# Kernel tuning notes

Hardware: AMD Instinct MI355X
Metric: run time of the kernel (lower is better)

The kernel has to match this reference:

```python
import jax, jax.numpy as jnp
import numpy as np
import math

B, H, L = 8, 512, 2048
CH = 1          # channels
D2 = 32         # d_state // 2 (conjugate pairs)
DT_MIN, DT_MAX = 0.001, 0.1


def setup_inputs() -> dict:
    key = jax.random.key(0)
    ks = jax.random.split(key, 7)
    u = jax.random.normal(ks[0], (B, H, L), dtype=jnp.float32)
    # Chebyshev initialization (SimpleS4)
    h_scale = jnp.exp(jnp.arange(H, dtype=jnp.float32) / H * math.log(DT_MAX / DT_MIN))
    angles = jnp.arange(D2, dtype=jnp.float32) * jnp.pi
    theta = jnp.broadcast_to(angles[None, None, :], (CH, H, D2)).astype(jnp.float32) + 0.0
    a = -(jnp.broadcast_to(h_scale[None, :, None], (CH, H, D2)).astype(jnp.float32) + 0.0)
    b = jax.random.normal(ks[1], (CH, H, D2), dtype=jnp.float32)
    c = jax.random.normal(ks[2], (CH, H, D2), dtype=jnp.float32)
    x0 = jax.random.normal(ks[3], (CH, H, D2), dtype=jnp.float32)
    D = jax.random.normal(ks[4], (CH, H), dtype=jnp.float32)
    lim = 1.0 / math.sqrt(CH * H)
    W = jax.random.uniform(ks[5], (H, CH * H), minval=-lim, maxval=lim, dtype=jnp.float32)
    bias = jax.random.uniform(ks[6], (H,), minval=-lim, maxval=lim, dtype=jnp.float32)
    return dict(u=u, a=a, theta=theta, b=b, c=c, x0=x0, D=D, W=W, bias=bias)


def fft_conv(u, f):
    # u: (B,H,L), f: (C,H,L) -> causal conv (B,C,H,L) via zero-padded FFT
    n = 2 * u.shape[-1]
    u_f = jnp.fft.rfft(u, n=n)
    f_f = jnp.fft.rfft(f, n=n)
    y = jnp.fft.irfft(jnp.einsum('bhl,chl->bchl', u_f, f_f), n=n)
    return y[..., : u.shape[-1]]


def s4_forward(u, a, theta, b, c, x0, D, W, bias):
    Bsz, Hd, l = u.shape
    T = 1.0 / (l - 1)                                   # quadrature step
    z = T * jnp.arange(l, dtype=u.dtype)                # (L,)
    aa = -jnp.abs(a)                                    # (C,H,D2) stable decay
    # Vandermonde-like basis: exp(a z) cos(theta z), shape (C,H,D2,L)
    base = jnp.exp(aa[..., None] * z) * jnp.cos(theta[..., None] * z)
    q = b * c                                           # (C,H,D2)
    f = 2.0 * T * jnp.einsum('chd,chdl->chl', q, base)  # SSM kernel (C,H,L)
    y = fft_conv(u, f)                                  # (B,C,H,L)
    # trapezoid-rule endpoint correction
    y = y - 0.5 * (jnp.einsum('ch,bhl->bchl', f[:, :, 0], u)
                   + jnp.einsum('chl,bh->bchl', f, u[:, :, 0]))
    # initial-state contribution (x0 term)
    k0 = 2.0 * jnp.einsum('chd,chdl->chl', c * x0, base)
    y = y + k0[None]
    # skip connection D*u
    y = y + jnp.einsum('ch,bhl->bchl', D, u)
    y = y.reshape(Bsz, CH * Hd, l)                      # (B, C*H, L)
    # NonLinear head: GELU -> pointwise Linear(C*H -> H) (transposed conv1x1)
    y = jax.nn.gelu(y, approximate=False)
    out = jnp.einsum('hf,bfl->bhl', W, y) + bias[None, :, None]
    return out


def reference(u, a, theta, b, c, x0, D, W, bias):
    return s4_forward(u, a, theta, b, c, x0, D, W, bias)
```

## Files before the change

### kernel.cpp

```cpp
#include <hip/hip_runtime.h>
#include <hip/hip_bf16.h>

#define B_  8
#define H_  512
#define L_  2048
#define D2_ 32
#define NC_ 64
#define LC_ 32
#define EP  36

typedef __attribute__((ext_vector_type(8))) short short8;
typedef __attribute__((ext_vector_type(8))) _Float16 half8;
typedef __attribute__((ext_vector_type(2))) _Float16 half2v;
typedef __attribute__((ext_vector_type(4))) float float4v;

__device__ __forceinline__ half2v pk_fma16(half2v a, half2v b, half2v c) {
    return __builtin_elementwise_fma(a, b, c);
}

__device__ __forceinline__ float gelu_fast(float x) {
    float q = x * fmaf(0.044715f, x * x, 1.0f);
    float s = __expf(-1.5957691216057308f * q);
    return __fdividef(x, 1.0f + s);
}

__device__ __forceinline__ unsigned pack_bf16x2(float x, float y) {
    __hip_bfloat162 p = __float22bfloat162_rn(make_float2(x, y));
    return *(unsigned*)&p;
}
__device__ __forceinline__ float2 unpack_bf16x2(unsigned v) {
    __hip_bfloat162 p = *(__hip_bfloat162*)&v;
    return __bfloat1622float2(p);
}
__device__ __forceinline__ unsigned pack_f16x2(float x, float y) {
    auto v = __builtin_amdgcn_cvt_pkrtz(x, y);
    return *(unsigned*)&v;
}

__device__ __forceinline__ void load_lds16(const void* g, void* l) {
    __builtin_amdgcn_global_load_lds((const __attribute__((address_space(1))) unsigned int*)g,
                                     (__attribute__((address_space(3))) unsigned int*)l, 16, 0, 0);
}

__global__ void cast_prep_kernel(const float* __restrict__ W, __hip_bfloat16* __restrict__ Wb,
                                 const float* __restrict__ a, const float* __restrict__ th,
                                 const float* __restrict__ bb, const float* __restrict__ cc,
                                 const float* __restrict__ x0,
                                 float* __restrict__ aT, float* __restrict__ thT,
                                 float* __restrict__ qT, float* __restrict__ gxT,
                                 _Float16* __restrict__ WPh) {
    int tid = blockIdx.x * 256 + threadIdx.x;
    Wb[tid] = __float2bfloat16(W[tid]);
    if (tid < H_ * D2_) {
        int h = tid & (H_ - 1);
        int d = tid >> 9;
        const float T = 1.0f / (float)(L_ - 1);
        float av = -fabsf(a[h * D2_ + d]);
        float tv = th[h * D2_ + d];
        float q  = bb[h * D2_ + d] * cc[h * D2_ + d];
        aT[tid]  = av;
        thT[tid] = tv;
        qT[tid]  = q;
        gxT[tid] = 2.0f * cc[h * D2_ + d] * x0[h * D2_ + d];
        #pragma unroll
        for (int k = 0; k < 6; ++k) {
            float len = (float)(32 << k);
            float e2  = __expf(av * T * len);
            float an  = tv * T * len;
            WPh[((size_t)h * 6 + k) * 64 + d]      = (_Float16)(e2 * __cosf(an));
            WPh[((size_t)h * 6 + k) * 64 + 32 + d] = (_Float16)(e2 * __sinf(an));
        }
    }
}

__global__ __launch_bounds__(256) void fkprep_kernel(
        const float* __restrict__ aT, const float* __restrict__ thT,
        const float* __restrict__ qT, const float* __restrict__ gxT,
        unsigned* __restrict__ FKf, _Float16* __restrict__ AB,
        _Float16* __restrict__ CB) {
    __shared__ float f_lds[32];
    int h = blockIdx.x;
    int t = threadIdx.x;
    int q4 = t & 3, lc = t >> 2;
    const float T = 1.0f / (float)(L_ - 1);
    float z0 = T * (float)(lc * 32);
    float pr[8], pi[8], wr[8], wi[8], qd[8], gx[8];
    #pragma unroll
    for (int j = 0; j < 8; ++j) {
        int idx = (q4 * 8 + j) * H_ + h;
        float aa = aT[idx], tv = thT[idx];
        float e0 = __expf(aa * z0);
        pr[j] = e0 * __cosf(tv * z0);
        pi[j] = e0 * __sinf(tv * z0);
        float e1 = __expf(aa * T);
        wr[j] = e1 * __cosf(tv * T);
        wi[j] = e1 * __sinf(tv * T);
        qd[j] = qT[idx];
        gx[j] = gxT[idx];
    }
    for (int i = 0; i < 32; ++i) {
        float fa = 0.f, ka = 0.f;
        #pragma unroll
        for (int j = 0; j < 8; ++j) {
            fa = fmaf(qd[j], pr[j], fa);
            ka = fmaf(gx[j], pr[j], ka);
            float nr = fmaf(pr[j], wr[j], -(pi[j] * wi[j]));
            float ni = fmaf(pr[j], wi[j],  (pi[j] * wr[j]));
            pr[j] = nr; pi[j] = ni;
        }
        fa += __shfl_xor(fa, 1); fa += __shfl_xor(fa, 2);
        ka += __shfl_xor(ka, 1); ka += __shfl_xor(ka, 2);
        if (q4 == 0) {
            float fv = 2.0f * T * fa;
            FKf[(size_t)h * L_ + lc * 32 + i] = pack_bf16x2(fv, ka);
            if (lc == 0) f_lds[i] = fv;
        }
    }
    __syncthreads();
    for (int e = t; e < 64 * 32; e += 256) {
        int m = e >> 5, i = e & 31;
        int d = m & 31;
        float av = aT[d * H_ + h], tv = thT[d * H_ + h];
        float z  = T * (float)(31 - i);
        float ex = __expf(av * z);
        float v  = (m < 32) ? ex * __cosf(tv * z) : ex * __sinf(tv * z);
        AB[(size_t)h * 2048 + e] = (_Float16)v;
    }
    for (int e = t; e < 32 * 96; e += 256) {
        int i = e / 96, k = e - i * 96;
        float v = 0.f;
        if (k < 32) {
            if (k <= i) v = f_lds[i - k];
        } else {
            int d = (k < 64) ? k - 32 : k - 64;
            float av = aT[d * H_ + h], tv = thT[d * H_ + h];
            float qs = 2.0f * T * qT[d * H_ + h];
            float z  = T * (float)(i + 1);
            float ex = __expf(av * z);
            v = (k < 64) ? qs * ex * __cosf(tv * z) : -qs * ex * __sinf(tv * z);
        }
        CB[(size_t)h * 3072 + e] = (_Float16)v;
    }
}

__global__ __launch_bounds__(128, 6) void scan_mfma_kernel(
        const float* __restrict__ u, const _Float16* __restrict__ AB,
        const _Float16* __restrict__ CB, const unsigned* __restrict__ WPh,
        const float* __restrict__ Dp, const unsigned* __restrict__ FKf,
        __hip_bfloat16* __restrict__ y) {
    __shared__ __align__(16) unsigned El[64 * EP];
    int wid = threadIdx.x >> 6, lane = threadIdx.x & 63;
    int h = blockIdx.x, b = blockIdx.y;
    int ln = lane & 15, qq = lane >> 4;
    const float* ug = u + (size_t)(b * H_ + h) * L_;

    half8 uf[4];
    #pragma unroll
    for (int nb = 0; nb < 4; ++nb) {
        const float* p = ug + (nb * 16 + ln) * 32 + qq * 8;
        float4 a0 = *(const float4*)p;
        float4 a1 = *(const float4*)(p + 4);
        unsigned* vp = (unsigned*)&uf[nb];
        vp[0] = pack_f16x2(a0.x, a0.y);
        vp[1] = pack_f16x2(a0.z, a0.w);
        vp[2] = pack_f16x2(a1.x, a1.y);
        vp[3] = pack_f16x2(a1.z, a1.w);
    }

    const _Float16* ABh = AB + (size_t)h * 2048;
    int j0 = wid * 8 + qq * 2;
    #pragma unroll
    for (int e = 0; e < 2; ++e) {
        half8 af = *(const half8*)&ABh[(e * 32 + wid * 16 + ln) * 32 + qq * 8];
        #pragma unroll
        for (int nb = 0; nb < 4; ++nb) {
            float4v acc = (float4v){0.f, 0.f, 0.f, 0.f};
            acc = __builtin_amdgcn_mfma_f32_16x16x32_f16(af, uf[nb], acc, 0, 0, 0);
            unsigned p0 = pack_f16x2(acc[0], acc[1]);
            unsigned p1 = pack_f16x2(acc[2], acc[3]);
            *(uint2*)&El[(nb * 16 + ln) * EP + e * 16 + j0] = make_uint2(p0, p1);
        }
    }
    asm volatile("s_waitcnt lgkmcnt(0)" ::: "memory");
    __builtin_amdgcn_sched_barrier(0);

    int c = lane;
    unsigned sr[8], si[8];
    {
        const unsigned* rp = &El[c * EP + wid * 8];
        uint4 r0 = *(const uint4*)rp;
        uint4 r1 = *(const uint4*)(rp + 4);
        uint4 i0 = *(const uint4*)(rp + 16);
        uint4 i1 = *(const uint4*)(rp + 20);
        sr[0]=r0.x; sr[1]=r0.y; sr[2]=r0.z; sr[3]=r0.w;
        sr[4]=r1.x; sr[5]=r1.y; sr[6]=r1.z; sr[7]=r1.w;
        si[0]=i0.x; si[1]=i0.y; si[2]=i0.z; si[3]=i0.w;
        si[4]=i1.x; si[5]=i1.y; si[6]=i1.z; si[7]=i1.w;
    }
    const unsigned* mpb = WPh + (size_t)h * 6 * 32;
    #pragma unroll
    for (int st = 0; st < 6; ++st) {
        int off = 1 << st;
        int src = (c - off) & 63;
        bool act = c >= off;
        const unsigned* mp = mpb + st * 32 + wid * 8;
        #pragma unroll
        for (int jj = 0; jj < 8; ++jj) {
            unsigned prp = (unsigned)__shfl((int)sr[jj], src);
            unsigned pip = (unsigned)__shfl((int)si[jj], src);
            if (!act) { prp = 0u; pip = 0u; }
            unsigned mru = mp[jj];
            unsigned miu = mp[16 + jj];
            unsigned min_ = miu ^ 0x80008000u;
            half2v pr = *(half2v*)&prp, pi = *(half2v*)&pip;
            half2v Mr = *(half2v*)&mru, Mi = *(half2v*)&miu, Mni = *(half2v*)&min_;
            half2v s_r = *(half2v*)&sr[jj], s_i = *(half2v*)&si[jj];
            half2v nr = pk_fma16(pr, Mr, pk_fma16(pi, Mni, s_r));
            half2v ni = pk_fma16(pr, Mi, pk_fma16(pi, Mr,  s_i));
            sr[jj] = *(unsigned*)&nr; si[jj] = *(unsigned*)&ni;
        }
    }
    {
        int srcm1 = (c - 1) & 63;
        #pragma unroll
        for (int jj = 0; jj < 8; ++jj) {
            unsigned a0 = (unsigned)__shfl((int)sr[jj], srcm1);
            unsigned b0 = (unsigned)__shfl((int)si[jj], srcm1);
            if (c == 0) { a0 = 0u; b0 = 0u; }
            sr[jj] = a0; si[jj] = b0;
        }
    }
    {
        unsigned* wp = &El[c * EP + wid * 8];
        *(uint4*)wp        = make_uint4(sr[0], sr[1], sr[2], sr[3]);
        *(uint4*)(wp + 4)  = make_uint4(sr[4], sr[5], sr[6], sr[7]);
        *(uint4*)(wp + 16) = make_uint4(si[0], si[1], si[2], si[3]);
        *(uint4*)(wp + 20) = make_uint4(si[4], si[5], si[6], si[7]);
    }
    const unsigned* fgh = FKf + (size_t)h * L_;
    uint4 fkp[2][2];
    #pragma unroll
    for (int nbi = 0; nbi < 2; ++nbi) {
        int col = (2 * wid + nbi) * 16 + ln;
        fkp[nbi][0] = *(const uint4*)&fgh[col * 32 + qq * 4];
        fkp[nbi][1] = *(const uint4*)&fgh[col * 32 + 16 + qq * 4];
    }
    __syncthreads();

    const _Float16* CBh = CB + (size_t)h * 3072;
    float4v acc2[2][2];
    #pragma unroll
    for (int mb = 0; mb < 2; ++mb)
        #pragma unroll
        for (int nbi = 0; nbi < 2; ++nbi)
            acc2[mb][nbi] = (float4v){0.f, 0.f, 0.f, 0.f};
    #pragma unroll
    for (int ks = 0; ks < 3; ++ks) {
        half8 a2[2];
        a2[0] = *(const half8*)&CBh[(ln)      * 96 + ks * 32 + qq * 8];
        a2[1] = *(const half8*)&CBh[(16 + ln) * 96 + ks * 32 + qq * 8];
        #pragma unroll
        for (int nbi = 0; nbi < 2; ++nbi) {
            int col = (2 * wid + nbi) * 16 + ln;
            half8 bfv;
            if (ks == 0) bfv = uf[2 * wid + nbi];
            else {
                int off = (ks == 1) ? 0 : 16;
                bfv = *(const half8*)&El[col * EP + off + qq * 4];
            }
            acc2[0][nbi] = __builtin_amdgcn_mfma_f32_16x16x32_f16(a2[0], bfv, acc2[0][nbi], 0, 0, 0);
            acc2[1][nbi] = __builtin_amdgcn_mfma_f32_16x16x32_f16(a2[1], bfv, acc2[1][nbi], 0, 0, 0);
        }
    }

    float f0; { f0 = unpack_bf16x2(fgh[0]).x; }
    float c0v = Dp[h] - 0.5f * f0;
    float c1v = -0.5f * ug[0];
    #pragma unroll
    for (int nbi = 0; nbi < 2; ++nbi) {
        int col = (2 * wid + nbi) * 16 + ln;
        #pragma unroll
        for (int mb = 0; mb < 2; ++mb) {
            int l0 = col * 32 + mb * 16 + qq * 4;
            float4 u4 = *(const float4*)(ug + l0);
            uint4 fkv = fkp[nbi][mb];
            float us[4] = {u4.x, u4.y, u4.z, u4.w};
            unsigned fs[4] = {fkv.x, fkv.y, fkv.z, fkv.w};
            float g[4];
            #pragma unroll
            for (int r = 0; r < 4; ++r) {
                float2 fk = unpack_bf16x2(fs[r]);
                float yv = acc2[mb][nbi][r] + fmaf(c0v, us[r], fmaf(c1v, fk.x, fk.y));
                g[r] = gelu_fast(yv);
            }
            uint2 yo;
            yo.x = pack_bf16x2(g[0], g[1]);
            yo.y = pack_bf16x2(g[2], g[3]);
            *(uint2*)((short*)y + (size_t)(b * H_ + h) * L_ + l0) = yo;
        }
    }
}

__global__ __launch_bounds__(256) void transpose_y_kernel(
        const __hip_bfloat16* __restrict__ y, __hip_bfloat16* __restrict__ yT) {
    __shared__ short tile[64][72];
    int l0 = blockIdx.x * 64, f0 = blockIdx.y * 64, b = blockIdx.z;
    int t = threadIdx.x;
    int row = t >> 3, col8 = (t & 7) * 8;
    const short* yg = (const short*)y + (size_t)b * H_ * L_;
    #pragma unroll
    for (int r2 = 0; r2 < 64; r2 += 32)
        *(uint4*)&tile[row + r2][col8] =
            *(const uint4*)&yg[(size_t)(f0 + row + r2) * L_ + l0 + col8];
    __syncthreads();
    short* og = (short*)yT + (size_t)b * L_ * H_;
    #pragma unroll
    for (int r2 = 0; r2 < 64; r2 += 32) {
        int lrow = row + r2;
        short v[8];
        #pragma unroll
        for (int j = 0; j < 8; ++j) v[j] = tile[col8 + j][lrow];
        *(uint4*)&og[(size_t)(l0 + lrow) * H_ + f0 + col8] = *(uint4*)v;
    }
}

__global__ __launch_bounds__(256) void gemm_kernel(
        const __hip_bfloat16* __restrict__ Wb, const __hip_bfloat16* __restrict__ yT,
        const float* __restrict__ bias, float* __restrict__ out) {
    __shared__ __align__(16) short As[64 * 32];
    __shared__ __align__(16) short Bs[128 * 32];
    int l0 = blockIdx.x * 128;
    int h0 = blockIdx.y * 64;
    int b  = blockIdx.z;
    int t    = threadIdx.x;
    int lane = t & 63, wave = t >> 6;
    int m_off = (wave >> 1) * 32, n_off = (wave & 1) * 64;
    int quad = lane >> 4, ln = lane & 15;

    float4v acc[2][4];
    #pragma unroll
    for (int mt = 0; mt < 2; ++mt)
        #pragma unroll
        for (int nt = 0; nt < 4; ++nt)
            acc[mt][nt] = (float4v){0.f, 0.f, 0.f, 0.f};

    const short* Wg = (const short*)Wb;
    const short* Yg = (const short*)(yT + (size_t)b * L_ * H_);

    int r  = t >> 2;
    int qd = t & 3;

    for (int kt = 0; kt < 16; ++kt) {
        int k0 = kt * 32;
        load_lds16(Wg + (h0 + r) * 512 + k0 + qd * 8, &As[t * 8]);
        load_lds16(Yg + (size_t)(l0 + r)      * 512 + k0 + qd * 8, &Bs[t * 8]);
        load_lds16(Yg + (size_t)(l0 + r + 64) * 512 + k0 + qd * 8, &Bs[(t + 256) * 8]);
        __syncthreads();

        short8 af[2], bf[4];
        #pragma unroll
        for (int mt = 0; mt < 2; ++mt)
            af[mt] = *(const short8*)&As[(m_off + mt * 16 + ln) * 32 + quad * 8];
        #pragma unroll
        for (int nt = 0; nt < 4; ++nt)
            bf[nt] = *(const short8*)&Bs[(n_off + nt * 16 + ln) * 32 + quad * 8];
        #pragma unroll
        for (int mt = 0; mt < 2; ++mt)
            #pragma unroll
            for (int nt = 0; nt < 4; ++nt)
                acc[mt][nt] = __builtin_amdgcn_mfma_f32_16x16x32_bf16(
                    af[mt], bf[nt], acc[mt][nt], 0, 0, 0);
        __syncthreads();
    }

    #pragma unroll
    for (int mt = 0; mt < 2; ++mt) {
        #pragma unroll
        for (int nt = 0; nt < 4; ++nt) {
            int hh = h0 + m_off + mt * 16 + quad * 4;
            int ll = l0 + n_off + nt * 16 + ln;
            #pragma unroll
            for (int r2 = 0; r2 < 4; ++r2)
                out[((size_t)(b * H_ + hh + r2)) * L_ + ll] = acc[mt][nt][r2] + bias[hh + r2];
        }
    }
}

extern "C" void kernel_launch(void* const* d_in, const int* in_sizes, int n_in,
                              void* d_out, int out_size, void* d_ws, size_t ws_size,
                              hipStream_t stream) {
    const float* u    = (const float*)d_in[0];
    const float* a    = (const float*)d_in[1];
    const float* th   = (const float*)d_in[2];
    const float* bb   = (const float*)d_in[3];
    const float* cc   = (const float*)d_in[4];
    const float* x0   = (const float*)d_in[5];
    const float* Dp   = (const float*)d_in[6];
    const float* W    = (const float*)d_in[7];
    const float* bias = (const float*)d_in[8];
    float* out = (float*)d_out;
    char* ws = (char*)d_ws;

    unsigned*       FKf = (unsigned*)ws;
    __hip_bfloat16* yT  = (__hip_bfloat16*)(ws + (4ull  << 20));
    __hip_bfloat16* y   = (__hip_bfloat16*)(ws + (20ull << 20));
    __hip_bfloat16* Wb  = (__hip_bfloat16*)(ws + (36ull << 20));
    _Float16*       AB  = (_Float16*)(ws + (37ull << 20));
    _Float16*       CB  = (_Float16*)(ws + (39ull << 20));
    float* pbase = (float*)(ws + (42ull << 20));
    float *aT  = pbase,           *thT = pbase + 16384, *qT = pbase + 2*16384,
          *gxT = pbase + 3*16384;
    _Float16* WPh = (_Float16*)(pbase + 4*16384);

    hipLaunchKernelGGL(cast_prep_kernel,  dim3(1024),      dim3(256), 0, stream,
                       W, Wb, a, th, bb, cc, x0, aT, thT, qT, gxT, WPh);
    hipLaunchKernelGGL(fkprep_kernel,     dim3(H_),        dim3(256), 0, stream,
                       aT, thT, qT, gxT, FKf, AB, CB);
    hipLaunchKernelGGL(scan_mfma_kernel,  dim3(H_, B_),    dim3(128), 0, stream,
                       u, AB, CB, (const unsigned*)WPh, Dp, FKf, y);
    hipLaunchKernelGGL(transpose_y_kernel,dim3(32, 8, 8),  dim3(256), 0, stream, y, yT);
    hipLaunchKernelGGL(gemm_kernel,       dim3(16, 8, 8),  dim3(256), 0, stream,
                       Wb, yT, bias, out);
}
```

Before: 171.9 us.

## Process two batches per scan block and XOR-swizzle transpose LDS tile

The scan kernel now handles two batch elements per block, reusing the per-channel AB/CB matrices, scan multipliers and FK loads across both batches and halving the grid. Launch bounds drop to 4 waves to leave room for the doubled register state. Separately, the transpose kernel XOR-swizzles its shared tile columns so the column-wise reads hit fewer LDS bank conflicts. The trade-off is higher register and LDS use per block and fewer blocks in flight for latency hiding.

```diff
diff --git a/kernel.cpp b/kernel.cpp
--- a/kernel.cpp
+++ b/kernel.cpp
@@ -143,28 +143,34 @@
     }
 }
 
-__global__ __launch_bounds__(128, 6) void scan_mfma_kernel(
+__global__ __launch_bounds__(128, 4) void scan_mfma_kernel(
         const float* __restrict__ u, const _Float16* __restrict__ AB,
         const _Float16* __restrict__ CB, const unsigned* __restrict__ WPh,
         const float* __restrict__ Dp, const unsigned* __restrict__ FKf,
         __hip_bfloat16* __restrict__ y) {
-    __shared__ __align__(16) unsigned El[64 * EP];
+    __shared__ __align__(16) unsigned El[2][64 * EP];
     int wid = threadIdx.x >> 6, lane = threadIdx.x & 63;
-    int h = blockIdx.x, b = blockIdx.y;
+    int h = blockIdx.x, b0 = blockIdx.y * 2;
     int ln = lane & 15, qq = lane >> 4;
-    const float* ug = u + (size_t)(b * H_ + h) * L_;
-
-    half8 uf[4];
-    #pragma unroll
-    for (int nb = 0; nb < 4; ++nb) {
-        const float* p = ug + (nb * 16 + ln) * 32 + qq * 8;
-        float4 a0 = *(const float4*)p;
-        float4 a1 = *(const float4*)(p + 4);
-        unsigned* vp = (unsigned*)&uf[nb];
-        vp[0] = pack_f16x2(a0.x, a0.y);
-        vp[1] = pack_f16x2(a0.z, a0.w);
-        vp[2] = pack_f16x2(a1.x, a1.y);
-        vp[3] = pack_f16x2(a1.z, a1.w);
+    const float* ug[2] = { u + (size_t)(b0 * H_ + h) * L_,
+                           u + (size_t)((b0 + 1) * H_ + h) * L_ };
+
+    half8 uf[2][4];
+    float u0[2];
+    #pragma unroll
+    for (int bi = 0; bi < 2; ++bi) {
+        u0[bi] = ug[bi][0];
+        #pragma unroll
+        for (int nb = 0; nb < 4; ++nb) {
+            const float* p = ug[bi] + (nb * 16 + ln) * 32 + qq * 8;
+            float4 a0 = *(const float4*)p;
+            float4 a1 = *(const float4*)(p + 4);
+            unsigned* vp = (unsigned*)&uf[bi][nb];
+            vp[0] = pack_f16x2(a0.x, a0.y);
+            vp[1] = pack_f16x2(a0.z, a0.w);
+            vp[2] = pack_f16x2(a1.x, a1.y);
+            vp[3] = pack_f16x2(a1.z, a1.w);
+        }
     }
 
     const _Float16* ABh = AB + (size_t)h * 2048;
@@ -173,29 +179,31 @@
     for (int e = 0; e < 2; ++e) {
         half8 af = *(const half8*)&ABh[(e * 32 + wid * 16 + ln) * 32 + qq * 8];
         #pragma unroll
-        for (int nb = 0; nb < 4; ++nb) {
-            float4v acc = (float4v){0.f, 0.f, 0.f, 0.f};
-            acc = __builtin_amdgcn_mfma_f32_16x16x32_f16(af, uf[nb], acc, 0, 0, 0);
-            unsigned p0 = pack_f16x2(acc[0], acc[1]);
-            unsigned p1 = pack_f16x2(acc[2], acc[3]);
-            *(uint2*)&El[(nb * 16 + ln) * EP + e * 16 + j0] = make_uint2(p0, p1);
-        }
+        for (int bi = 0; bi < 2; ++bi)
+            #pragma unroll
+            for (int nb = 0; nb < 4; ++nb) {
+                float4v acc = (float4v){0.f, 0.f, 0.f, 0.f};
+                acc = __builtin_amdgcn_mfma_f32_16x16x32_f16(af, uf[bi][nb], acc, 0, 0, 0);
+                *(uint2*)&El[bi][(nb * 16 + ln) * EP + e * 16 + j0] =
+                    make_uint2(pack_f16x2(acc[0], acc[1]), pack_f16x2(acc[2], acc[3]));
+            }
     }
     asm volatile("s_waitcnt lgkmcnt(0)" ::: "memory");
     __builtin_amdgcn_sched_barrier(0);
 
     int c = lane;
-    unsigned sr[8], si[8];
-    {
-        const unsigned* rp = &El[c * EP + wid * 8];
+    unsigned sr[2][8], si[2][8];
+    #pragma unroll
+    for (int bi = 0; bi < 2; ++bi) {
+        const unsigned* rp = &El[bi][c * EP + wid * 8];
         uint4 r0 = *(const uint4*)rp;
         uint4 r1 = *(const uint4*)(rp + 4);
         uint4 i0 = *(const uint4*)(rp + 16);
         uint4 i1 = *(const uint4*)(rp + 20);
-        sr[0]=r0.x; sr[1]=r0.y; sr[2]=r0.z; sr[3]=r0.w;
-        sr[4]=r1.x; sr[5]=r1.y; sr[6]=r1.z; sr[7]=r1.w;
-        si[0]=i0.x; si[1]=i0.y; si[2]=i0.z; si[3]=i0.w;
-        si[4]=i1.x; si[5]=i1.y; si[6]=i1.z; si[7]=i1.w;
+        sr[bi][0]=r0.x; sr[bi][1]=r0.y; sr[bi][2]=r0.z; sr[bi][3]=r0.w;
+        sr[bi][4]=r1.x; sr[bi][5]=r1.y; sr[bi][6]=r1.z; sr[bi][7]=r1.w;
+        si[bi][0]=i0.x; si[bi][1]=i0.y; si[bi][2]=i0.z; si[bi][3]=i0.w;
+        si[bi][4]=i1.x; si[bi][5]=i1.y; si[bi][6]=i1.z; si[bi][7]=i1.w;
     }
     const unsigned* mpb = WPh + (size_t)h * 6 * 32;
     #pragma unroll
@@ -206,36 +214,42 @@
         const unsigned* mp = mpb + st * 32 + wid * 8;
         #pragma unroll
         for (int jj = 0; jj < 8; ++jj) {
-            unsigned prp = (unsigned)__shfl((int)sr[jj], src);
-            unsigned pip = (unsigned)__shfl((int)si[jj], src);
-            if (!act) { prp = 0u; pip = 0u; }
             unsigned mru = mp[jj];
             unsigned miu = mp[16 + jj];
             unsigned min_ = miu ^ 0x80008000u;
-            half2v pr = *(half2v*)&prp, pi = *(half2v*)&pip;
-            half2v Mr = *(half2v*)&mru, Mi = *(half2v*)&miu, Mni = *(half2v*)&min_;
-            half2v s_r = *(half2v*)&sr[jj], s_i = *(half2v*)&si[jj];
-            half2v nr = pk_fma16(pr, Mr, pk_fma16(pi, Mni, s_r));
-            half2v ni = pk_fma16(pr, Mi, pk_fma16(pi, Mr,  s_i));
-            sr[jj] = *(unsigned*)&nr; si[jj] = *(unsigned*)&ni;
+            #pragma unroll
+            for (int bi = 0; bi < 2; ++bi) {
+                unsigned prp = (unsigned)__shfl((int)sr[bi][jj], src);
+                unsigned pip = (unsigned)__shfl((int)si[bi][jj], src);
+                if (!act) { prp = 0u; pip = 0u; }
+                half2v pr = *(half2v*)&prp, pi = *(half2v*)&pip;
+                half2v Mr = *(half2v*)&mru, Mi = *(half2v*)&miu, Mni = *(half2v*)&min_;
+                half2v s_r = *(half2v*)&sr[bi][jj], s_i = *(half2v*)&si[bi][jj];
+                half2v nr = pk_fma16(pr, Mr, pk_fma16(pi, Mni, s_r));
+                half2v ni = pk_fma16(pr, Mi, pk_fma16(pi, Mr,  s_i));
+                sr[bi][jj] = *(unsigned*)&nr; si[bi][jj] = *(unsigned*)&ni;
+            }
         }
     }
     {
         int srcm1 = (c - 1) & 63;
         #pragma unroll
-        for (int jj = 0; jj < 8; ++jj) {
-            unsigned a0 = (unsigned)__shfl((int)sr[jj], srcm1);
-            unsigned b0 = (unsigned)__shfl((int)si[jj], srcm1);
-            if (c == 0) { a0 = 0u; b0 = 0u; }
-            sr[jj] = a0; si[jj] = b0;
-        }
-    }
-    {
-        unsigned* wp = &El[c * EP + wid * 8];
-        *(uint4*)wp        = make_uint4(sr[0], sr[1], sr[2], sr[3]);
-        *(uint4*)(wp + 4)  = make_uint4(sr[4], sr[5], sr[6], sr[7]);
-        *(uint4*)(wp + 16) = make_uint4(si[0], si[1], si[2], si[3]);
-        *(uint4*)(wp + 20) = make_uint4(si[4], si[5], si[6], si[7]);
+        for (int bi = 0; bi < 2; ++bi)
+            #pragma unroll
+            for (int jj = 0; jj < 8; ++jj) {
+                unsigned a0 = (unsigned)__shfl((int)sr[bi][jj], srcm1);
+                unsigned b1 = (unsigned)__shfl((int)si[bi][jj], srcm1);
+                if (c == 0) { a0 = 0u; b1 = 0u; }
+                sr[bi][jj] = a0; si[bi][jj] = b1;
+            }
+    }
+    #pragma unroll
+    for (int bi = 0; bi < 2; ++bi) {
+        unsigned* wp = &El[bi][c * EP + wid * 8];
+        *(uint4*)wp        = make_uint4(sr[bi][0], sr[bi][1], sr[bi][2], sr[bi][3]);
+        *(uint4*)(wp + 4)  = make_uint4(sr[bi][4], sr[bi][5], sr[bi][6], sr[bi][7]);
+        *(uint4*)(wp + 16) = make_uint4(si[bi][0], si[bi][1], si[bi][2], si[bi][3]);
+        *(uint4*)(wp + 20) = make_uint4(si[bi][4], si[bi][5], si[bi][6], si[bi][7]);
     }
     const unsigned* fgh = FKf + (size_t)h * L_;
     uint4 fkp[2][2];
@@ -248,55 +262,57 @@
     __syncthreads();
 
     const _Float16* CBh = CB + (size_t)h * 3072;
-    float4v acc2[2][2];
-    #pragma unroll
-    for (int mb = 0; mb < 2; ++mb)
-        #pragma unroll
-        for (int nbi = 0; nbi < 2; ++nbi)
-            acc2[mb][nbi] = (float4v){0.f, 0.f, 0.f, 0.f};
-    #pragma unroll
-    for (int ks = 0; ks < 3; ++ks) {
-        half8 a2[2];
-        a2[0] = *(const half8*)&CBh[(ln)      * 96 + ks * 32 + qq * 8];
-        a2[1] = *(const half8*)&CBh[(16 + ln) * 96 + ks * 32 + qq * 8];
+    float f0; { f0 = unpack_bf16x2(fgh[0]).x; }
+    float c0v = Dp[h] - 0.5f * f0;
+    #pragma unroll
+    for (int bi = 0; bi < 2; ++bi) {
+        float c1v = -0.5f * u0[bi];
+        float4v acc2[2][2];
+        #pragma unroll
+        for (int mb = 0; mb < 2; ++mb)
+            #pragma unroll
+            for (int nbi = 0; nbi < 2; ++nbi)
+                acc2[mb][nbi] = (float4v){0.f, 0.f, 0.f, 0.f};
+        #pragma unroll
+        for (int ks = 0; ks < 3; ++ks) {
+            half8 a2[2];
+            a2[0] = *(const half8*)&CBh[(ln)      * 96 + ks * 32 + qq * 8];
+            a2[1] = *(const half8*)&CBh[(16 + ln) * 96 + ks * 32 + qq * 8];
+            #pragma unroll
+            for (int nbi = 0; nbi < 2; ++nbi) {
+                int col = (2 * wid + nbi) * 16 + ln;
+                half8 bfv;
+                if (ks == 0) bfv = uf[bi][2 * wid + nbi];
+                else {
+                    int off = (ks == 1) ? 0 : 16;
+                    bfv = *(const half8*)&El[bi][col * EP + off + qq * 4];
+                }
+                acc2[0][nbi] = __builtin_amdgcn_mfma_f32_16x16x32_f16(a2[0], bfv, acc2[0][nbi], 0, 0, 0);
+                acc2[1][nbi] = __builtin_amdgcn_mfma_f32_16x16x32_f16(a2[1], bfv, acc2[1][nbi], 0, 0, 0);
+            }
+        }
         #pragma unroll
         for (int nbi = 0; nbi < 2; ++nbi) {
             int col = (2 * wid + nbi) * 16 + ln;
-            half8 bfv;
-            if (ks == 0) bfv = uf[2 * wid + nbi];
-            else {
-                int off = (ks == 1) ? 0 : 16;
-                bfv = *(const half8*)&El[col * EP + off + qq * 4];
+            #pragma unroll
+            for (int mb = 0; mb < 2; ++mb) {
+                int l0 = col * 32 + mb * 16 + qq * 4;
+                float4 u4 = *(const float4*)(ug[bi] + l0);
+                uint4 fkv = fkp[nbi][mb];
+                float us[4] = {u4.x, u4.y, u4.z, u4.w};
+                unsigned fs[4] = {fkv.x, fkv.y, fkv.z, fkv.w};
+                float g[4];
+                #pragma unroll
+                for (int r = 0; r < 4; ++r) {
+                    float2 fk = unpack_bf16x2(fs[r]);
+                    float yv = acc2[mb][nbi][r] + fmaf(c0v, us[r], fmaf(c1v, fk.x, fk.y));
+                    g[r] = gelu_fast(yv);
+                }
+                uint2 yo;
+                yo.x = pack_bf16x2(g[0], g[1]);
+                yo.y = pack_bf16x2(g[2], g[3]);
+                *(uint2*)((short*)y + (size_t)((b0 + bi) * H_ + h) * L_ + l0) = yo;
             }
-            acc2[0][nbi] = __builtin_amdgcn_mfma_f32_16x16x32_f16(a2[0], bfv, acc2[0][nbi], 0, 0, 0);
-            acc2[1][nbi] = __builtin_amdgcn_mfma_f32_16x16x32_f16(a2[1], bfv, acc2[1][nbi], 0, 0, 0);
-        }
-    }
-
-    float f0; { f0 = unpack_bf16x2(fgh[0]).x; }
-    float c0v = Dp[h] - 0.5f * f0;
-    float c1v = -0.5f * ug[0];
-    #pragma unroll
-    for (int nbi = 0; nbi < 2; ++nbi) {
-        int col = (2 * wid + nbi) * 16 + ln;
-        #pragma unroll
-        for (int mb = 0; mb < 2; ++mb) {
-            int l0 = col * 32 + mb * 16 + qq * 4;
-            float4 u4 = *(const float4*)(ug + l0);
-            uint4 fkv = fkp[nbi][mb];
-            float us[4] = {u4.x, u4.y, u4.z, u4.w};
-            unsigned fs[4] = {fkv.x, fkv.y, fkv.z, fkv.w};
-            float g[4];
-            #pragma unroll
-            for (int r = 0; r < 4; ++r) {
-                float2 fk = unpack_bf16x2(fs[r]);
-                float yv = acc2[mb][nbi][r] + fmaf(c0v, us[r], fmaf(c1v, fk.x, fk.y));
-                g[r] = gelu_fast(yv);
-            }
-            uint2 yo;
-            yo.x = pack_bf16x2(g[0], g[1]);
-            yo.y = pack_bf16x2(g[2], g[3]);
-            *(uint2*)((short*)y + (size_t)(b * H_ + h) * L_ + l0) = yo;
         }
     }
 }
@@ -309,9 +325,11 @@
     int row = t >> 3, col8 = (t & 7) * 8;
     const short* yg = (const short*)y + (size_t)b * H_ * L_;
     #pragma unroll
-    for (int r2 = 0; r2 < 64; r2 += 32)
-        *(uint4*)&tile[row + r2][col8] =
-            *(const uint4*)&yg[(size_t)(f0 + row + r2) * L_ + l0 + col8];
+    for (int r2 = 0; r2 < 64; r2 += 32) {
+        int fr = row + r2;
+        *(uint4*)&tile[fr][col8 ^ (8 * ((fr >> 3) & 7))] =
+            *(const uint4*)&yg[(size_t)(f0 + fr) * L_ + l0 + col8];
+    }
     __syncthreads();
     short* og = (short*)yT + (size_t)b * L_ * H_;
     #pragma unroll
@@ -319,7 +337,10 @@
         int lrow = row + r2;
         short v[8];
         #pragma unroll
-        for (int j = 0; j < 8; ++j) v[j] = tile[col8 + j][lrow];
+        for (int j = 0; j < 8; ++j) {
+            int f = col8 + j;
+            v[j] = tile[f][lrow ^ (8 * ((f >> 3) & 7))];
+        }
         *(uint4*)&og[(size_t)(l0 + lrow) * H_ + f0 + col8] = *(uint4*)v;
     }
 }
@@ -416,7 +437,7 @@
                        W, Wb, a, th, bb, cc, x0, aT, thT, qT, gxT, WPh);
     hipLaunchKernelGGL(fkprep_kernel,     dim3(H_),        dim3(256), 0, stream,
                        aT, thT, qT, gxT, FKf, AB, CB);
-    hipLaunchKernelGGL(scan_mfma_kernel,  dim3(H_, B_),    dim3(128), 0, stream,
+    hipLaunchKernelGGL(scan_mfma_kernel,  dim3(H_, B_/2),  dim3(128), 0, stream,
                        u, AB, CB, (const unsigned*)WPh, Dp, FKf, y);
     hipLaunchKernelGGL(transpose_y_kernel,dim3(32, 8, 8),  dim3(256), 0, stream, y, yT);
     hipLaunchKernelGGL(gemm_kernel,       dim3(16, 8, 8),  dim3(256), 0, stream,
```

New measurement: 194.5 us. 1.13x slower.
